# Performance work log

Measured on AMD Instinct MI355X. Metric: run time of the kernel, lower is better.

Reference implementation:

```python
import math
import jax, jax.numpy as jnp
import numpy as np

S, D = 4096, 2048
H, DH = 16, 128
ROPE_BASE = 10000.0


def _rotate_half(x):
    # x: [..., dh]; pairs (x1, x2) -> (-x2, x1), interleaved
    shp = x.shape
    x = x.reshape(*shp[:-1], shp[-1] // 2, 2)
    x1, x2 = x[..., 0], x[..., 1]
    return jnp.stack((-x2, x1), axis=-1).reshape(shp)


def _rope_cos_sin(seq_len, dh):
    inv_freq = 1.0 / (ROPE_BASE ** (jnp.arange(0, dh, 2, dtype=jnp.float32) / dh))
    t = jnp.arange(seq_len, dtype=jnp.float32)
    freqs = jnp.einsum('i,j->ij', t, inv_freq)  # [S, dh/2]
    cos = jnp.repeat(jnp.cos(freqs), 2, axis=-1)  # [S, dh]
    sin = jnp.repeat(jnp.sin(freqs), 2, axis=-1)
    return cos, sin


def setup_inputs() -> dict:
    key = jax.random.key(0)
    kx, kq, kk, kv, ko = jax.random.split(key, 5)
    scale_in = 1.0 / math.sqrt(D)
    scale_hd = 1.0 / math.sqrt(H * DH)
    return {
        'x': jax.random.normal(kx, (S, D), dtype=jnp.float32),
        'mask': jnp.tril(jnp.ones((S, S), dtype=bool)),  # causal
        'wq': jax.random.normal(kq, (H * DH, D), dtype=jnp.float32) * scale_in,
        'wk': jax.random.normal(kk, (H * DH, D), dtype=jnp.float32) * scale_in,
        'wv': jax.random.normal(kv, (H * DH, D), dtype=jnp.float32) * scale_in,
        'wo': jax.random.normal(ko, (D, H * DH), dtype=jnp.float32) * scale_hd,
    }


def reference(x, mask, wq, wk, wv, wo):
    s = x.shape[0]
    # QKV projections (Linear: y = W @ x per token) -> [h, S, dh]
    q = (x @ wq.T).reshape(s, H, DH).transpose(1, 0, 2)
    k = (x @ wk.T).reshape(s, H, DH).transpose(1, 0, 2)
    v = (x @ wv.T).reshape(s, H, DH).transpose(1, 0, 2)
    # RoPE
    cos, sin = _rope_cos_sin(s, DH)  # [S, dh] each
    q = q * cos[None] + _rotate_half(q) * sin[None]
    k = k * cos[None] + _rotate_half(k) * sin[None]
    # Attention
    sim = jnp.einsum('hid,hjd->hij', q, k) / math.sqrt(DH)  # [h, S, S]
    sim = jnp.where(mask[None], sim, -jnp.inf)
    attn = jax.nn.softmax(sim, axis=-1)
    out = jnp.einsum('hij,hjd->ihd', attn, v).reshape(s, H * DH)
    return out @ wo.T
```

## Files before the change

kernel.cpp:

```cpp
#include <hip/hip_runtime.h>
#include <stdint.h>

#define S_LEN 4096
#define D_MODEL 2048
#define NH 16
#define DH 128

typedef short s16x8 __attribute__((ext_vector_type(8)));
typedef short s16x2 __attribute__((ext_vector_type(2)));
typedef unsigned short u16;
typedef unsigned short u16x4 __attribute__((ext_vector_type(4)));
typedef float f32x4 __attribute__((ext_vector_type(4)));

__device__ __forceinline__ u16 f2bf(float f) {
  union { float f; uint32_t u; } v; v.f = f;
  uint32_t u = v.u;
  u += 0x7FFFu + ((u >> 16) & 1u);
  return (u16)(u >> 16);
}

__device__ __forceinline__ float bf2f(u16 b) {
  union { uint32_t u; float f; } v; v.u = ((uint32_t)b) << 16;
  return v.f;
}

__device__ __forceinline__ void async_copy16(const u16* g, u16* l) {
  __builtin_amdgcn_global_load_lds(
      (const __attribute__((address_space(1))) unsigned int*)g,
      (__attribute__((address_space(3))) unsigned int*)l, 16, 0, 0);
}

__global__ void cast_kernel(const float4* __restrict__ src, u16* __restrict__ dst, int n4) {
  int i = blockIdx.x * blockDim.x + threadIdx.x;
  if (i >= n4) return;
  float4 v = src[i];
  u16x4 o;
  o[0] = f2bf(v.x); o[1] = f2bf(v.y); o[2] = f2bf(v.z); o[3] = f2bf(v.w);
  *(u16x4*)(dst + (size_t)i * 4) = o;
}

__global__ void cast4_kernel(const float4* __restrict__ s0, const float4* __restrict__ s1,
                             const float4* __restrict__ s2, const float4* __restrict__ s3,
                             u16* __restrict__ d0, u16* __restrict__ d1,
                             u16* __restrict__ d2, u16* __restrict__ d3) {
  int b = blockIdx.x;
  int which = b >> 12;
  const float4* src = which == 0 ? s0 : which == 1 ? s1 : which == 2 ? s2 : s3;
  u16* dst = which == 0 ? d0 : which == 1 ? d1 : which == 2 ? d2 : d3;
  int i = (b & 4095) * blockDim.x + threadIdx.x;
  float4 v = src[i];
  u16x4 o;
  o[0] = f2bf(v.x); o[1] = f2bf(v.y); o[2] = f2bf(v.z); o[3] = f2bf(v.w);
  *(u16x4*)(dst + (size_t)i * 4) = o;
}

__global__ void rope_table(float* __restrict__ ctab, float* __restrict__ stab) {
  int idx = blockIdx.x * blockDim.x + threadIdx.x;
  int t = idx >> 6, p = idx & 63;
  float invf = powf(10000.0f, -(float)p / 64.0f);
  float th = (float)t * invf;
  ctab[idx] = cosf(th);
  stab[idx] = sinf(th);
}

#define PH_LGK0() do { asm volatile("s_waitcnt lgkmcnt(0)" ::: "memory"); \
                       __builtin_amdgcn_sched_barrier(0); } while (0)

__device__ __forceinline__ void stage16k(const u16* __restrict__ src, u16* dstbase,
                                         const int K) {
  const int tid = threadIdx.x;
  int rr = tid >> 3;
  int gc = ((tid & 7) ^ (rr & 7)) << 3;
  const u16* s = src + (size_t)rr * K + gc;
  u16* d = dstbase + (tid << 3);
  async_copy16(s, d);
  async_copy16(s + (size_t)64 * K, d + 4096);
}

__device__ __forceinline__ void mma256x128(
    const u16* __restrict__ Ab, const u16* __restrict__ Bb,
    const int K, u16* lds, f32x4 (&acc)[4][4])
{
  const int tid = threadIdx.x;
  const int lane = tid & 63, quad = lane >> 4, l16 = lane & 15;
  const int w = tid >> 6, wr = w >> 1, wc = w & 1;

  u16* const A0 = lds;
  u16* const B0 = lds + 16384;
  u16* const A1 = lds + 24576;
  u16* const B1 = lds + 40960;
  const int NT = K >> 6;

  auto sA = [&](int t, u16* buf) {
    int tc = t < NT ? t : NT - 1;
    stage16k(Ab + ((size_t)tc << 6), buf, K);
    stage16k(Ab + (size_t)128 * K + ((size_t)tc << 6), buf + 8192, K);
  };
  auto sB = [&](int t, u16* buf) {
    int tc = t < NT ? t : NT - 1;
    stage16k(Bb + ((size_t)tc << 6), buf, K);
  };

  s16x8 aC[4][2], aN[4][2], bA[2][2], bB0[2][2], bB1[2][2];

  auto rdA = [&](const u16* buf, s16x8 (&a)[4][2]) {
#pragma unroll
    for (int mt = 0; mt < 4; ++mt) {
      int ra = (wr << 6) + (mt << 4) + l16;
#pragma unroll
      for (int ks = 0; ks < 2; ++ks)
        a[mt][ks] = *(const s16x8*)(buf + (ra << 6) + ((((ks << 2) + quad) ^ (ra & 7)) << 3));
    }
  };
  auto rdBh = [&](const u16* buf, int nh, s16x8 (&b)[2][2]) {
#pragma unroll
    for (int nt = 0; nt < 2; ++nt) {
      int rb = (wc << 6) + (((nh << 1) + nt) << 4) + l16;
#pragma unroll
      for (int ks = 0; ks < 2; ++ks)
        b[nt][ks] = *(const s16x8*)(buf + (rb << 6) + ((((ks << 2) + quad) ^ (rb & 7)) << 3));
    }
  };
  auto mmah = [&](s16x8 (&a)[4][2], s16x8 (&b)[2][2], int nh) {
#pragma unroll
    for (int mt = 0; mt < 4; ++mt)
#pragma unroll
      for (int nt = 0; nt < 2; ++nt)
#pragma unroll
        for (int ks = 0; ks < 2; ++ks)
          acc[mt][(nh << 1) + nt] = __builtin_amdgcn_mfma_f32_16x16x32_bf16(
              a[mt][ks], b[nt][ks], acc[mt][(nh << 1) + nt], 0, 0, 0);
  };

  sA(0, A0); sB(0, B0); sA(1, A1); sB(1, B1);
  asm volatile("s_waitcnt vmcnt(6)" ::: "memory");
  __builtin_amdgcn_s_barrier();
  rdA(A0, aC); rdBh(B0, 0, bA); rdBh(B0, 1, bB0);

  const int NI = K >> 7;
#pragma unroll 1
  for (int i = 0; i < NI; ++i) {
    const int t0 = 2 * i, t1 = 2 * i + 1;
    __builtin_amdgcn_s_barrier();
    PH_LGK0();
    __builtin_amdgcn_s_setprio(1);
    mmah(aC, bA, 0);
    __builtin_amdgcn_s_setprio(0);
    asm volatile("s_waitcnt vmcnt(0)" ::: "memory");
    __builtin_amdgcn_s_barrier();
    __builtin_amdgcn_s_barrier();
    PH_LGK0();
    __builtin_amdgcn_s_setprio(1);
    sA(t0 + 2, A0); sB(t0 + 2, B0);
    rdA(A1, aN); rdBh(B1, 0, bA); rdBh(B1, 1, bB1);
    mmah(aC, bB0, 1);
    __builtin_amdgcn_s_setprio(0);
    __builtin_amdgcn_s_barrier();
    __builtin_amdgcn_s_barrier();
    PH_LGK0();
    __builtin_amdgcn_s_setprio(1);
    mmah(aN, bA, 0);
    __builtin_amdgcn_s_setprio(0);
    asm volatile("s_waitcnt vmcnt(0)" ::: "memory");
    __builtin_amdgcn_s_barrier();
    __builtin_amdgcn_s_barrier();
    PH_LGK0();
    __builtin_amdgcn_s_setprio(1);
    sA(t1 + 2, A1); sB(t1 + 2, B1);
    if (i + 1 < NI) { rdA(A0, aC); rdBh(B0, 0, bA); rdBh(B0, 1, bB0); }
    mmah(aN, bB1, 1);
    __builtin_amdgcn_s_setprio(0);
    __builtin_amdgcn_s_barrier();
  }
}

__global__ __launch_bounds__(512) void gemm256_qkv(
    const u16* __restrict__ A,
    const u16* __restrict__ wqb, const u16* __restrict__ wkb, const u16* __restrict__ wvb,
    u16* __restrict__ qh, u16* __restrict__ kh, u16* __restrict__ vh,
    const float* __restrict__ ctab, const float* __restrict__ stab)
{
  __shared__ __align__(16) u16 lds[49152];
  const int tid = threadIdx.x;
  const int lane = tid & 63, quad = lane >> 4, l16 = lane & 15;
  const int w = tid >> 6, wr = w >> 1, wc = w & 1;
  const int m0 = blockIdx.x << 8;
  const int by = blockIdx.y;
  const int which = by >> 4;
  const int n0 = (by & 15) << 7;
  const u16* B = which == 0 ? wqb : which == 1 ? wkb : wvb;
  u16* outp = which == 0 ? qh : which == 1 ? kh : vh;

  f32x4 acc[4][4];
  f32x4 zero = {0.f, 0.f, 0.f, 0.f};
#pragma unroll
  for (int i = 0; i < 4; ++i)
#pragma unroll
    for (int j = 0; j < 4; ++j) acc[i][j] = zero;

  mma256x128(A + (size_t)m0 * D_MODEL, B + (size_t)n0 * D_MODEL, D_MODEL, lds, acc);

#pragma unroll
  for (int mt = 0; mt < 4; ++mt) {
    int rowg = m0 + (wr << 6) + (mt << 4) + (quad << 2);
#pragma unroll
    for (int nt = 0; nt < 4; ++nt) {
      int cl = n0 + (wc << 6) + (nt << 4) + l16;
      int hh = cl >> 7, dd = cl & 127;
      int p = dd >> 1;
      f32x4 v = acc[mt][nt];
#pragma unroll
      for (int r = 0; r < 4; ++r) {
        float val = v[r];
        if (which < 2) {
          float partner = __shfl_xor(val, 1);
          float c = ctab[(size_t)(rowg + r) * 64 + p];
          float s = stab[(size_t)(rowg + r) * 64 + p];
          val = (dd & 1) ? fmaf(val, c, partner * s) : fmaf(val, c, -partner * s);
        }
        outp[((size_t)hh * S_LEN + (rowg + r)) * DH + dd] = f2bf(val);
      }
    }
  }
}

__global__ __launch_bounds__(512) void gemm256_out(
    const u16* __restrict__ A, const u16* __restrict__ B, float* __restrict__ outF)
{
  __shared__ __align__(16) u16 lds[49152];
  const int tid = threadIdx.x;
  const int lane = tid & 63, quad = lane >> 4, l16 = lane & 15;
  const int w = tid >> 6, wr = w >> 1, wc = w & 1;
  const int m0 = blockIdx.x << 8, n0 = blockIdx.y << 7;

  f32x4 acc[4][4];
  f32x4 zero = {0.f, 0.f, 0.f, 0.f};
#pragma unroll
  for (int i = 0; i < 4; ++i)
#pragma unroll
    for (int j = 0; j < 4; ++j) acc[i][j] = zero;

  mma256x128(A + (size_t)m0 * D_MODEL, B + (size_t)n0 * D_MODEL, D_MODEL, lds, acc);

#pragma unroll
  for (int mt = 0; mt < 4; ++mt) {
    int rowg = m0 + (wr << 6) + (mt << 4) + (quad << 2);
#pragma unroll
    for (int nt = 0; nt < 4; ++nt) {
      int col = n0 + (wc << 6) + (nt << 4) + l16;
      f32x4 v = acc[mt][nt];
#pragma unroll
      for (int r = 0; r < 4; ++r) outF[(size_t)(rowg + r) * D_MODEL + col] = v[r];
    }
  }
}

__global__ __launch_bounds__(512) void attn_kernel(
    const u16* __restrict__ Q, const u16* __restrict__ Kb,
    const u16* __restrict__ V,
    u16* __restrict__ U0, u16* __restrict__ U1, float* __restrict__ lbuf)
{
  __shared__ __align__(16) u16 lk[2][64 * 128];
  __shared__ __align__(16) u16 lvt[2][128 * 64];
  __shared__ __align__(16) u16 lp[8 * 2048];

  const int tid = threadIdx.x;
  const int w = tid >> 6, lane = tid & 63, quad = lane >> 4, l16 = lane & 15;
  const int linear = blockIdx.x;
  const int slot = linear >> 3;
  const int h = ((linear & 7) << 1) | (slot >> 4);
  const int bx = slot & 15;

  const u16* Qh = Q + (size_t)h * S_LEN * DH;
  const u16* Kh = Kb + (size_t)h * S_LEN * DH;
  const u16* Vh = V + (size_t)h * S_LEN * DH;

  const float scale = 0.08838834764831845f;
  const s16x8 vones = {0x3F80, 0x3F80, 0x3F80, 0x3F80, 0x3F80, 0x3F80, 0x3F80, 0x3F80};
  f32x4 zero = {0.f, 0.f, 0.f, 0.f};
  u16* lpw = lp + (w << 11);

  for (int seg = 0; seg < 2; ++seg) {
    const int qt = seg ? bx : (15 - bx);
    const int jlo = seg ? (2 * qt + 2) : 0;
    const int jhi = seg ? (4 * qt + 4) : (2 * qt + 2);
    const int i0 = qt << 8;
    const int iws = i0 + (w << 5);

    s16x8 qf[2][4];
#pragma unroll
    for (int s = 0; s < 2; ++s)
#pragma unroll
      for (int ks = 0; ks < 4; ++ks)
        qf[s][ks] = *(const s16x8*)(Qh + (size_t)(iws + (s << 4) + l16) * DH + ks * 32 + quad * 8);

    f32x4 accO[2][8];
#pragma unroll
    for (int s = 0; s < 2; ++s)
#pragma unroll
      for (int dt = 0; dt < 8; ++dt) accO[s][dt] = zero;
    f32x4 accL[2] = {zero, zero};

    {
      const int j0 = jlo << 6;
      int u = tid & 31, c8 = tid >> 5, r0 = u << 1;
      s16x8 v0 = *(const s16x8*)(Vh + (size_t)(j0 + r0) * DH + (c8 << 3));
      s16x8 v1 = *(const s16x8*)(Vh + (size_t)(j0 + r0 + 1) * DH + (c8 << 3));
#pragma unroll
      for (int rnd = 0; rnd < 2; ++rnd) {
        int c = rnd * 512 + tid;
        int r = c >> 4, cc = c & 15;
        int gcol = ((cc ^ (r & 15)) << 3);
        async_copy16(Kh + (size_t)(j0 + r) * DH + gcol, lk[0] + ((rnd * 512 + w * 64) << 3));
      }
      int cc = r0 >> 3;
#pragma unroll
      for (int e = 0; e < 8; ++e) {
        int d = (c8 << 3) + e;
        int off = (d << 6) + ((cc ^ (d & 7)) << 3) + (r0 & 7);
        s16x2 pr = {v0[e], v1[e]};
        *(s16x2*)(lvt[0] + off) = pr;
      }
    }
    __syncthreads();

    int cur = 0;
    for (int jt = jlo; jt < jhi; ++jt) {
      const int j0 = jt << 6;
      const bool has_next = (jt + 1) < jhi;

      s16x8 nv0, nv1;
      if (has_next) {
        const int nj0 = (jt + 1) << 6;
        int u = tid & 31, c8 = tid >> 5, r0 = u << 1;
        nv0 = *(const s16x8*)(Vh + (size_t)(nj0 + r0) * DH + (c8 << 3));
        nv1 = *(const s16x8*)(Vh + (size_t)(nj0 + r0 + 1) * DH + (c8 << 3));
#pragma unroll
        for (int rnd = 0; rnd < 2; ++rnd) {
          int c = rnd * 512 + tid;
          int r = c >> 4, cc = c & 15;
          int gcol = ((cc ^ (r & 15)) << 3);
          async_copy16(Kh + (size_t)(nj0 + r) * DH + gcol,
                       lk[cur ^ 1] + ((rnd * 512 + w * 64) << 3));
        }
      }

      const u16* lkc = lk[cur];
      f32x4 sa[2][4];
#pragma unroll
      for (int s = 0; s < 2; ++s)
#pragma unroll
        for (int nt = 0; nt < 4; ++nt) sa[s][nt] = zero;
      __builtin_amdgcn_s_setprio(1);
#pragma unroll
      for (int ks = 0; ks < 4; ++ks) {
#pragma unroll
        for (int nt = 0; nt < 4; ++nt) {
          int row = (nt << 4) + l16;
          s16x8 kf = *(const s16x8*)(lkc + (row << 7) + ((((ks << 2) + quad) ^ (row & 15)) << 3));
          sa[0][nt] = __builtin_amdgcn_mfma_f32_16x16x32_bf16(qf[0][ks], kf, sa[0][nt], 0, 0, 0);
          sa[1][nt] = __builtin_amdgcn_mfma_f32_16x16x32_bf16(qf[1][ks], kf, sa[1][nt], 0, 0, 0);
        }
      }
      __builtin_amdgcn_s_setprio(0);

#pragma unroll
      for (int s = 0; s < 2; ++s) {
        const int iw = iws + (s << 4);
        const bool maskt = (j0 + 63 > iw);
        u16* lps = lpw + (s << 10);
#pragma unroll
        for (int nt = 0; nt < 4; ++nt) {
          int col = (nt << 4) + l16;
          int j = j0 + col;
          int ccp = col >> 3;
#pragma unroll
          for (int r = 0; r < 4; ++r) {
            float raw = sa[s][nt][r];
            if (maskt) {
              int i = iw + (quad << 2) + r;
              if (j > i) raw = -1.0e30f;
            }
            float p = __expf(fmaf(raw, scale, -8.0f));
            union { float f; uint32_t u; } pv; pv.f = p;
            int m = (quad << 2) + r;
            lps[(m << 6) + ((ccp ^ (m & 7)) << 3) + (col & 7)] = (u16)(pv.u >> 16);
          }
        }
      }
      asm volatile("s_waitcnt lgkmcnt(0)" ::: "memory");
      s16x8 pf[2][2];
#pragma unroll
      for (int s = 0; s < 2; ++s)
#pragma unroll
        for (int kp = 0; kp < 2; ++kp)
          pf[s][kp] = *(const s16x8*)(lpw + (s << 10) + (l16 << 6) +
                                      ((((kp << 2) + quad) ^ (l16 & 7)) << 3));

      if (has_next) {
        int u = tid & 31, c8 = tid >> 5, r0 = u << 1;
        int cc = r0 >> 3;
        u16* dst = lvt[cur ^ 1];
#pragma unroll
        for (int e = 0; e < 8; ++e) {
          int d = (c8 << 3) + e;
          int off = (d << 6) + ((cc ^ (d & 7)) << 3) + (r0 & 7);
          s16x2 pr = {nv0[e], nv1[e]};
          *(s16x2*)(dst + off) = pr;
        }
      }

      const u16* lvc = lvt[cur];
      __builtin_amdgcn_s_setprio(1);
      accL[0] = __builtin_amdgcn_mfma_f32_16x16x32_bf16(pf[0][0], vones, accL[0], 0, 0, 0);
      accL[0] = __builtin_amdgcn_mfma_f32_16x16x32_bf16(pf[0][1], vones, accL[0], 0, 0, 0);
      accL[1] = __builtin_amdgcn_mfma_f32_16x16x32_bf16(pf[1][0], vones, accL[1], 0, 0, 0);
      accL[1] = __builtin_amdgcn_mfma_f32_16x16x32_bf16(pf[1][1], vones, accL[1], 0, 0, 0);
#pragma unroll
      for (int dt = 0; dt < 8; ++dt) {
#pragma unroll
        for (int kp = 0; kp < 2; ++kp) {
          int row = (dt << 4) + l16;
          s16x8 vf = *(const s16x8*)(lvc + (row << 6) + ((((kp << 2) + quad) ^ (row & 7)) << 3));
          accO[0][dt] = __builtin_amdgcn_mfma_f32_16x16x32_bf16(pf[0][kp], vf, accO[0][dt], 0, 0, 0);
          accO[1][dt] = __builtin_amdgcn_mfma_f32_16x16x32_bf16(pf[1][kp], vf, accO[1][dt], 0, 0, 0);
        }
      }
      __builtin_amdgcn_s_setprio(0);

      __syncthreads();
      cur ^= 1;
    }

    u16* Useg = seg ? U1 : U0;
    float* ls = lbuf + (size_t)seg * NH * S_LEN + (size_t)h * S_LEN;
#pragma unroll
    for (int s = 0; s < 2; ++s) {
      const int iw = iws + (s << 4);
#pragma unroll
      for (int r = 0; r < 4; ++r) {
        float lr = accL[s][r];
        float inv = lr > 0.f ? 1.0f / lr : 0.f;
        int srow = iw + (quad << 2) + r;
#pragma unroll
        for (int dt = 0; dt < 8; ++dt)
          Useg[((size_t)h * S_LEN + srow) * DH + (dt << 4) + l16] = f2bf(accO[s][dt][r] * inv);
        if (l16 == 0) ls[srow] = lr;
      }
    }
  }
}

__global__ void combine_kernel(const u16* __restrict__ U0, const u16* __restrict__ U1,
                               const float* __restrict__ lbuf, u16* __restrict__ ob)
{
  int t = blockIdx.x * 256 + threadIdx.x;
  int d8 = t & 15;
  int h = (t >> 4) & 15;
  int s = t >> 8;
  float l0 = lbuf[(size_t)h * S_LEN + s];
  float l1 = lbuf[(size_t)(NH * S_LEN) + (size_t)h * S_LEN + s];
  float inv = 1.0f / (l0 + l1);
  float w0 = l0 * inv, w1 = l1 * inv;
  size_t base = ((size_t)h * S_LEN + s) * DH + d8 * 8;
  s16x8 u0 = *(const s16x8*)(U0 + base);
  s16x8 u1 = *(const s16x8*)(U1 + base);
  u16 o[8];
#pragma unroll
  for (int e = 0; e < 8; ++e)
    o[e] = f2bf(w0 * bf2f((u16)u0[e]) + w1 * bf2f((u16)u1[e]));
  *(s16x8*)(ob + ((size_t)s * D_MODEL + h * DH + d8 * 8)) = *(s16x8*)o;
}

extern "C" void kernel_launch(void* const* d_in, const int* in_sizes, int n_in,
                              void* d_out, int out_size, void* d_ws, size_t ws_size,
                              hipStream_t stream) {
  const float* x  = (const float*)d_in[0];
  const float* wq = (const float*)d_in[2];
  const float* wk = (const float*)d_in[3];
  const float* wv = (const float*)d_in[4];
  const float* wo = (const float*)d_in[5];
  float* out = (float*)d_out;

  char* ws = (char*)d_ws;
  u16* xb  = (u16*)(ws);
  u16* wqb = (u16*)(ws + (16ull << 20));
  u16* wkb = (u16*)(ws + (24ull << 20));
  u16* wvb = (u16*)(ws + (32ull << 20));
  u16* wob = (u16*)(ws + (40ull << 20));
  u16* qh  = (u16*)(ws + (48ull << 20));
  u16* kh  = (u16*)(ws + (64ull << 20));
  u16* vh  = (u16*)(ws + (80ull << 20));
  float* ctab = (float*)(ws + (96ull << 20));
  float* stab = (float*)(ws + (97ull << 20));
  u16* U0 = (u16*)(ws);
  u16* U1 = (u16*)(ws + (16ull << 20));
  float* lbuf = (float*)(ws + (32ull << 20));
  u16* ob = qh;

  const int nx4 = S_LEN * D_MODEL / 4;
  cast_kernel<<<nx4 / 256, 256, 0, stream>>>((const float4*)x, xb, nx4);
  cast4_kernel<<<4 * 4096, 256, 0, stream>>>(
      (const float4*)wq, (const float4*)wk, (const float4*)wv, (const float4*)wo,
      wqb, wkb, wvb, wob);
  rope_table<<<(S_LEN * 64) / 256, 256, 0, stream>>>(ctab, stab);

  gemm256_qkv<<<dim3(S_LEN / 256, 3 * D_MODEL / 128), 512, 0, stream>>>(
      xb, wqb, wkb, wvb, qh, kh, vh, ctab, stab);

  attn_kernel<<<dim3(256), 512, 0, stream>>>(qh, kh, vh, U0, U1, lbuf);
  combine_kernel<<<S_LEN * NH * 16 / 256, 256, 0, stream>>>(U0, U1, lbuf, ob);

  gemm256_out<<<dim3(S_LEN / 256, D_MODEL / 128), 512, 0, stream>>>(
      ob, wob, out);
}
```

Before: 430.3 us.

## Switch GEMM mainloop to triple-buffered LDS with register double-buffering

```diff
diff --git a/kernel.cpp b/kernel.cpp
--- a/kernel.cpp
+++ b/kernel.cpp
@@ -63,9 +63,6 @@
   stab[idx] = sinf(th);
 }
 
-#define PH_LGK0() do { asm volatile("s_waitcnt lgkmcnt(0)" ::: "memory"); \
-                       __builtin_amdgcn_sched_barrier(0); } while (0)
-
 __device__ __forceinline__ void stage16k(const u16* __restrict__ src, u16* dstbase,
                                          const int K) {
   const int tid = threadIdx.x;
@@ -85,23 +82,17 @@
   const int lane = tid & 63, quad = lane >> 4, l16 = lane & 15;
   const int w = tid >> 6, wr = w >> 1, wc = w & 1;
 
-  u16* const A0 = lds;
-  u16* const B0 = lds + 16384;
-  u16* const A1 = lds + 24576;
-  u16* const B1 = lds + 40960;
+  u16* const B0 = lds;
+  u16* const B1 = lds + 24576;
+  u16* const B2 = lds + 49152;
   const int NT = K >> 6;
 
-  auto sA = [&](int t, u16* buf) {
+  auto sAB = [&](int t, u16* buf) {
     int tc = t < NT ? t : NT - 1;
     stage16k(Ab + ((size_t)tc << 6), buf, K);
     stage16k(Ab + (size_t)128 * K + ((size_t)tc << 6), buf + 8192, K);
+    stage16k(Bb + ((size_t)tc << 6), buf + 16384, K);
   };
-  auto sB = [&](int t, u16* buf) {
-    int tc = t < NT ? t : NT - 1;
-    stage16k(Bb + ((size_t)tc << 6), buf, K);
-  };
-
-  s16x8 aC[4][2], aN[4][2], bA[2][2], bB0[2][2], bB1[2][2];
 
   auto rdA = [&](const u16* buf, s16x8 (&a)[4][2]) {
 #pragma unroll
@@ -112,65 +103,61 @@
         a[mt][ks] = *(const s16x8*)(buf + (ra << 6) + ((((ks << 2) + quad) ^ (ra & 7)) << 3));
     }
   };
-  auto rdBh = [&](const u16* buf, int nh, s16x8 (&b)[2][2]) {
-#pragma unroll
-    for (int nt = 0; nt < 2; ++nt) {
-      int rb = (wc << 6) + (((nh << 1) + nt) << 4) + l16;
+  auto rdB = [&](const u16* buf, s16x8 (&b)[4][2]) {
+#pragma unroll
+    for (int nt = 0; nt < 4; ++nt) {
+      int rb = (wc << 6) + (nt << 4) + l16;
 #pragma unroll
       for (int ks = 0; ks < 2; ++ks)
-        b[nt][ks] = *(const s16x8*)(buf + (rb << 6) + ((((ks << 2) + quad) ^ (rb & 7)) << 3));
+        b[nt][ks] = *(const s16x8*)(buf + 16384 + (rb << 6) + ((((ks << 2) + quad) ^ (rb & 7)) << 3));
     }
   };
-  auto mmah = [&](s16x8 (&a)[4][2], s16x8 (&b)[2][2], int nh) {
+  auto mma32 = [&](s16x8 (&a)[4][2], s16x8 (&b)[4][2]) {
 #pragma unroll
     for (int mt = 0; mt < 4; ++mt)
 #pragma unroll
-      for (int nt = 0; nt < 2; ++nt)
+      for (int nt = 0; nt < 4; ++nt)
 #pragma unroll
         for (int ks = 0; ks < 2; ++ks)
-          acc[mt][(nh << 1) + nt] = __builtin_amdgcn_mfma_f32_16x16x32_bf16(
-              a[mt][ks], b[nt][ks], acc[mt][(nh << 1) + nt], 0, 0, 0);
+          acc[mt][nt] = __builtin_amdgcn_mfma_f32_16x16x32_bf16(
+              a[mt][ks], b[nt][ks], acc[mt][nt], 0, 0, 0);
   };
 
-  sA(0, A0); sB(0, B0); sA(1, A1); sB(1, B1);
-  asm volatile("s_waitcnt vmcnt(6)" ::: "memory");
+  s16x8 aE[4][2], bE[4][2], aO[4][2], bO[4][2];
+
+  sAB(0, B0); sAB(1, B1); sAB(2, B2);
+  asm volatile("s_waitcnt vmcnt(12)" ::: "memory");
   __builtin_amdgcn_s_barrier();
-  rdA(A0, aC); rdBh(B0, 0, bA); rdBh(B0, 1, bB0);
-
-  const int NI = K >> 7;
+  rdA(B0, aE); rdB(B0, bE);
+  asm volatile("s_waitcnt lgkmcnt(0)" ::: "memory");
+  __builtin_amdgcn_sched_barrier(0);
+
+  u16 *bc = B0, *bn = B1, *bs = B2;
 #pragma unroll 1
-  for (int i = 0; i < NI; ++i) {
-    const int t0 = 2 * i, t1 = 2 * i + 1;
+  for (int t = 0; t < NT; t += 2) {
     __builtin_amdgcn_s_barrier();
-    PH_LGK0();
+    sAB(t + 3, bc);
+    asm volatile("s_waitcnt vmcnt(12)" ::: "memory");
+    __builtin_amdgcn_s_barrier();
     __builtin_amdgcn_s_setprio(1);
-    mmah(aC, bA, 0);
+    if (t + 1 < NT) { rdA(bn, aO); rdB(bn, bO); }
+    mma32(aE, bE);
     __builtin_amdgcn_s_setprio(0);
-    asm volatile("s_waitcnt vmcnt(0)" ::: "memory");
+    asm volatile("s_waitcnt lgkmcnt(0)" ::: "memory");
+    __builtin_amdgcn_sched_barrier(0);
+    u16* tmp = bc; bc = bn; bn = bs; bs = tmp;
+
     __builtin_amdgcn_s_barrier();
+    sAB(t + 4, bc);
+    asm volatile("s_waitcnt vmcnt(12)" ::: "memory");
     __builtin_amdgcn_s_barrier();
-    PH_LGK0();
     __builtin_amdgcn_s_setprio(1);
-    sA(t0 + 2, A0); sB(t0 + 2, B0);
-    rdA(A1, aN); rdBh(B1, 0, bA); rdBh(B1, 1, bB1);
-    mmah(aC, bB0, 1);
+    if (t + 2 < NT) { rdA(bn, aE); rdB(bn, bE); }
+    mma32(aO, bO);
     __builtin_amdgcn_s_setprio(0);
-    __builtin_amdgcn_s_barrier();
-    __builtin_amdgcn_s_barrier();
-    PH_LGK0();
-    __builtin_amdgcn_s_setprio(1);
-    mmah(aN, bA, 0);
-    __builtin_amdgcn_s_setprio(0);
-    asm volatile("s_waitcnt vmcnt(0)" ::: "memory");
-    __builtin_amdgcn_s_barrier();
-    __builtin_amdgcn_s_barrier();
-    PH_LGK0();
-    __builtin_amdgcn_s_setprio(1);
-    sA(t1 + 2, A1); sB(t1 + 2, B1);
-    if (i + 1 < NI) { rdA(A0, aC); rdBh(B0, 0, bA); rdBh(B0, 1, bB0); }
-    mmah(aN, bB1, 1);
-    __builtin_amdgcn_s_setprio(0);
-    __builtin_amdgcn_s_barrier();
+    asm volatile("s_waitcnt lgkmcnt(0)" ::: "memory");
+    __builtin_amdgcn_sched_barrier(0);
+    tmp = bc; bc = bn; bn = bs; bs = tmp;
   }
 }
 
@@ -180,7 +167,7 @@
     u16* __restrict__ qh, u16* __restrict__ kh, u16* __restrict__ vh,
     const float* __restrict__ ctab, const float* __restrict__ stab)
 {
-  __shared__ __align__(16) u16 lds[49152];
+  __shared__ __align__(16) u16 lds[73728];
   const int tid = threadIdx.x;
   const int lane = tid & 63, quad = lane >> 4, l16 = lane & 15;
   const int w = tid >> 6, wr = w >> 1, wc = w & 1;
@@ -227,7 +214,7 @@
 __global__ __launch_bounds__(512) void gemm256_out(
     const u16* __restrict__ A, const u16* __restrict__ B, float* __restrict__ outF)
 {
-  __shared__ __align__(16) u16 lds[49152];
+  __shared__ __align__(16) u16 lds[73728];
   const int tid = threadIdx.x;
   const int lane = tid & 63, quad = lane >> 4, l16 = lane & 15;
   const int w = tid >> 6, wr = w >> 1, wc = w & 1;
```

Result: slower. 452.6 us (+5.2%).

## Halve attention block size to 128 query rows and single-buffer transposed V

Applied to the files above, without the earlier changes.

```diff
diff --git a/kernel.cpp b/kernel.cpp
--- a/kernel.cpp
+++ b/kernel.cpp
@@ -255,21 +255,21 @@
   }
 }
 
-__global__ __launch_bounds__(512) void attn_kernel(
+__global__ __launch_bounds__(256) void attn_kernel(
     const u16* __restrict__ Q, const u16* __restrict__ Kb,
     const u16* __restrict__ V,
     u16* __restrict__ U0, u16* __restrict__ U1, float* __restrict__ lbuf)
 {
   __shared__ __align__(16) u16 lk[2][64 * 128];
-  __shared__ __align__(16) u16 lvt[2][128 * 64];
-  __shared__ __align__(16) u16 lp[8 * 2048];
+  __shared__ __align__(16) u16 lvt[128 * 64];
+  __shared__ __align__(16) u16 lp[4 * 2048];
 
   const int tid = threadIdx.x;
   const int w = tid >> 6, lane = tid & 63, quad = lane >> 4, l16 = lane & 15;
   const int linear = blockIdx.x;
   const int slot = linear >> 3;
-  const int h = ((linear & 7) << 1) | (slot >> 4);
-  const int bx = slot & 15;
+  const int h = ((linear & 7) << 1) | (slot >> 5);
+  const int bx = slot & 31;
 
   const u16* Qh = Q + (size_t)h * S_LEN * DH;
   const u16* Kh = Kb + (size_t)h * S_LEN * DH;
@@ -280,11 +280,14 @@
   f32x4 zero = {0.f, 0.f, 0.f, 0.f};
   u16* lpw = lp + (w << 11);
 
+  const int vu = tid & 31, vc8 = tid >> 5, vr0 = vu << 1;
+  const int vccr = vr0 >> 3;
+
   for (int seg = 0; seg < 2; ++seg) {
-    const int qt = seg ? bx : (15 - bx);
-    const int jlo = seg ? (2 * qt + 2) : 0;
-    const int jhi = seg ? (4 * qt + 4) : (2 * qt + 2);
-    const int i0 = qt << 8;
+    const int qt = seg ? bx : (31 - bx);
+    const int jlo = seg ? (qt + 1) : 0;
+    const int jhi = seg ? (2 * qt + 2) : (qt + 1);
+    const int i0 = qt << 7;
     const int iws = i0 + (w << 5);
 
     s16x8 qf[2][4];
@@ -303,23 +306,27 @@
 
     {
       const int j0 = jlo << 6;
-      int u = tid & 31, c8 = tid >> 5, r0 = u << 1;
-      s16x8 v0 = *(const s16x8*)(Vh + (size_t)(j0 + r0) * DH + (c8 << 3));
-      s16x8 v1 = *(const s16x8*)(Vh + (size_t)(j0 + r0 + 1) * DH + (c8 << 3));
-#pragma unroll
-      for (int rnd = 0; rnd < 2; ++rnd) {
-        int c = rnd * 512 + tid;
+      s16x8 v0a = *(const s16x8*)(Vh + (size_t)(j0 + vr0) * DH + (vc8 << 4));
+      s16x8 v0b = *(const s16x8*)(Vh + (size_t)(j0 + vr0) * DH + (vc8 << 4) + 8);
+      s16x8 v1a = *(const s16x8*)(Vh + (size_t)(j0 + vr0 + 1) * DH + (vc8 << 4));
+      s16x8 v1b = *(const s16x8*)(Vh + (size_t)(j0 + vr0 + 1) * DH + (vc8 << 4) + 8);
+#pragma unroll
+      for (int rnd = 0; rnd < 4; ++rnd) {
+        int c = rnd * 256 + tid;
         int r = c >> 4, cc = c & 15;
         int gcol = ((cc ^ (r & 15)) << 3);
-        async_copy16(Kh + (size_t)(j0 + r) * DH + gcol, lk[0] + ((rnd * 512 + w * 64) << 3));
-      }
-      int cc = r0 >> 3;
+        async_copy16(Kh + (size_t)(j0 + r) * DH + gcol, lk[0] + ((rnd * 256 + w * 64) << 3));
+      }
 #pragma unroll
       for (int e = 0; e < 8; ++e) {
-        int d = (c8 << 3) + e;
-        int off = (d << 6) + ((cc ^ (d & 7)) << 3) + (r0 & 7);
-        s16x2 pr = {v0[e], v1[e]};
-        *(s16x2*)(lvt[0] + off) = pr;
+        int d = (vc8 << 4) + e;
+        int off = (d << 6) + ((vccr ^ (d & 7)) << 3) + (vr0 & 7);
+        s16x2 pr = {v0a[e], v1a[e]};
+        *(s16x2*)(lvt + off) = pr;
+        int d2 = d + 8;
+        int off2 = (d2 << 6) + ((vccr ^ (d2 & 7)) << 3) + (vr0 & 7);
+        s16x2 pr2 = {v0b[e], v1b[e]};
+        *(s16x2*)(lvt + off2) = pr2;
       }
     }
     __syncthreads();
@@ -329,19 +336,20 @@
       const int j0 = jt << 6;
       const bool has_next = (jt + 1) < jhi;
 
-      s16x8 nv0, nv1;
+      s16x8 nv0a, nv0b, nv1a, nv1b;
       if (has_next) {
         const int nj0 = (jt + 1) << 6;
-        int u = tid & 31, c8 = tid >> 5, r0 = u << 1;
-        nv0 = *(const s16x8*)(Vh + (size_t)(nj0 + r0) * DH + (c8 << 3));
-        nv1 = *(const s16x8*)(Vh + (size_t)(nj0 + r0 + 1) * DH + (c8 << 3));
-#pragma unroll
-        for (int rnd = 0; rnd < 2; ++rnd) {
-          int c = rnd * 512 + tid;
+        nv0a = *(const s16x8*)(Vh + (size_t)(nj0 + vr0) * DH + (vc8 << 4));
+        nv0b = *(const s16x8*)(Vh + (size_t)(nj0 + vr0) * DH + (vc8 << 4) + 8);
+        nv1a = *(const s16x8*)(Vh + (size_t)(nj0 + vr0 + 1) * DH + (vc8 << 4));
+        nv1b = *(const s16x8*)(Vh + (size_t)(nj0 + vr0 + 1) * DH + (vc8 << 4) + 8);
+#pragma unroll
+        for (int rnd = 0; rnd < 4; ++rnd) {
+          int c = rnd * 256 + tid;
           int r = c >> 4, cc = c & 15;
           int gcol = ((cc ^ (r & 15)) << 3);
           async_copy16(Kh + (size_t)(nj0 + r) * DH + gcol,
-                       lk[cur ^ 1] + ((rnd * 512 + w * 64) << 3));
+                       lk[cur ^ 1] + ((rnd * 256 + w * 64) << 3));
         }
       }
 
@@ -397,20 +405,6 @@
           pf[s][kp] = *(const s16x8*)(lpw + (s << 10) + (l16 << 6) +
                                       ((((kp << 2) + quad) ^ (l16 & 7)) << 3));
 
-      if (has_next) {
-        int u = tid & 31, c8 = tid >> 5, r0 = u << 1;
-        int cc = r0 >> 3;
-        u16* dst = lvt[cur ^ 1];
-#pragma unroll
-        for (int e = 0; e < 8; ++e) {
-          int d = (c8 << 3) + e;
-          int off = (d << 6) + ((cc ^ (d & 7)) << 3) + (r0 & 7);
-          s16x2 pr = {nv0[e], nv1[e]};
-          *(s16x2*)(dst + off) = pr;
-        }
-      }
-
-      const u16* lvc = lvt[cur];
       __builtin_amdgcn_s_setprio(1);
       accL[0] = __builtin_amdgcn_mfma_f32_16x16x32_bf16(pf[0][0], vones, accL[0], 0, 0, 0);
       accL[0] = __builtin_amdgcn_mfma_f32_16x16x32_bf16(pf[0][1], vones, accL[0], 0, 0, 0);
@@ -421,13 +415,27 @@
 #pragma unroll
         for (int kp = 0; kp < 2; ++kp) {
           int row = (dt << 4) + l16;
-          s16x8 vf = *(const s16x8*)(lvc + (row << 6) + ((((kp << 2) + quad) ^ (row & 7)) << 3));
+          s16x8 vf = *(const s16x8*)(lvt + (row << 6) + ((((kp << 2) + quad) ^ (row & 7)) << 3));
           accO[0][dt] = __builtin_amdgcn_mfma_f32_16x16x32_bf16(pf[0][kp], vf, accO[0][dt], 0, 0, 0);
           accO[1][dt] = __builtin_amdgcn_mfma_f32_16x16x32_bf16(pf[1][kp], vf, accO[1][dt], 0, 0, 0);
         }
       }
       __builtin_amdgcn_s_setprio(0);
 
+      __syncthreads();
+      if (has_next) {
+#pragma unroll
+        for (int e = 0; e < 8; ++e) {
+          int d = (vc8 << 4) + e;
+          int off = (d << 6) + ((vccr ^ (d & 7)) << 3) + (vr0 & 7);
+          s16x2 pr = {nv0a[e], nv1a[e]};
+          *(s16x2*)(lvt + off) = pr;
+          int d2 = d + 8;
+          int off2 = (d2 << 6) + ((vccr ^ (d2 & 7)) << 3) + (vr0 & 7);
+          s16x2 pr2 = {nv0b[e], nv1b[e]};
+          *(s16x2*)(lvt + off2) = pr2;
+        }
+      }
       __syncthreads();
       cur ^= 1;
     }
@@ -508,7 +516,7 @@
   gemm256_qkv<<<dim3(S_LEN / 256, 3 * D_MODEL / 128), 512, 0, stream>>>(
       xb, wqb, wkb, wvb, qh, kh, vh, ctab, stab);
 
-  attn_kernel<<<dim3(256), 512, 0, stream>>>(qh, kh, vh, U0, U1, lbuf);
+  attn_kernel<<<dim3(512), 256, 0, stream>>>(qh, kh, vh, U0, U1, lbuf);
   combine_kernel<<<S_LEN * NH * 16 / 256, 256, 0, stream>>>(U0, U1, lbuf, ob);
 
   gemm256_out<<<dim3(S_LEN / 256, D_MODEL / 128), 512, 0, stream>>>(
```

Result: slower. 504.5 us (+17.2%).
